# Kernel optimization log

Hardware: AMD Instinct MI355X
Metric: run time of the kernel (lower is better)

Reference implementation:

```python
import jax, jax.numpy as jnp
import numpy as np

D = 512
H = 8
DK = D // H
EPS = 1e-5

def _layer_norm(x, w, b):
    mu = jnp.mean(x, axis=-1, keepdims=True)
    var = jnp.mean(jnp.square(x - mu), axis=-1, keepdims=True)
    return (x - mu) * jax.lax.rsqrt(var + EPS) * w + b

def setup_inputs() -> dict:
    key = jax.random.key(0)
    ks = jax.random.split(key, 16)
    B, S = 4, 2048
    s = 1.0 / np.sqrt(D)
    inp = {
        'q': jax.random.normal(ks[0], (B, S, D), jnp.float32),
        'k': jax.random.normal(ks[1], (B, S, D), jnp.float32),
        'v': jax.random.normal(ks[2], (B, S, D), jnp.float32),
        'mask': jnp.ones((S, S), jnp.int32),
        'pos_k': jax.random.normal(ks[3], (S, S), jnp.float32),
        'ln_w': jnp.ones((D,), jnp.float32),
        'ln_b': jnp.zeros((D,), jnp.float32),
        'Wq': jax.random.uniform(ks[4], (D, D), jnp.float32, -s, s),
        'bq': jax.random.uniform(ks[5], (D,), jnp.float32, -s, s),
        'Wk': jax.random.uniform(ks[6], (D, D), jnp.float32, -s, s),
        'bk': jax.random.uniform(ks[7], (D,), jnp.float32, -s, s),
        'Wv': jax.random.uniform(ks[8], (D, D), jnp.float32, -s, s),
        'bv': jax.random.uniform(ks[9], (D,), jnp.float32, -s, s),
        'Wo': jax.random.uniform(ks[10], (D, D), jnp.float32, -s, s),
        'bo': jax.random.uniform(ks[11], (D,), jnp.float32, -s, s),
    }
    return inp

def reference(q, k, v, mask, pos_k, ln_w, ln_b, Wq, bq, Wk, bk, Wv, bv, Wo, bo):
    B, S, _ = q.shape
    # shared LayerNorm on q, k, v
    qn = _layer_norm(q, ln_w, ln_b)
    kn = _layer_norm(k, ln_w, ln_b)
    vn = _layer_norm(v, ln_w, ln_b)
    # projections -> [B, H, S, DK]
    qh = (qn @ Wq.T + bq).reshape(B, S, H, DK).transpose(0, 2, 1, 3)
    kh = (kn @ Wk.T + bk).reshape(B, S, H, DK).transpose(0, 2, 1, 3)
    vh = (vn @ Wv.T + bv).reshape(B, S, H, DK).transpose(0, 2, 1, 3)
    scores = jnp.einsum('bhqd,bhkd->bhqk', qh, kh) / np.sqrt(DK)
    scores = scores + pos_k[None, None, :S, :S]
    scores = jnp.where(mask[None, None] == 0, -jnp.inf, scores)
    attn = jax.nn.softmax(scores, axis=-1)  # dropout is identity in eval
    x = jnp.einsum('bhqk,bhkd->bhqd', attn, vh).transpose(0, 2, 1, 3).reshape(B, S, D)
    out = x @ Wo.T + bo
    return out, attn
```

## Files before the change

kernel.cpp:

```cpp
#include <hip/hip_runtime.h>


typedef __bf16 bf16;
typedef __attribute__((ext_vector_type(8))) __bf16 bfv8;
typedef __attribute__((ext_vector_type(4))) __bf16 bfv4;
typedef __attribute__((ext_vector_type(2))) __bf16 bfv2;
typedef __attribute__((ext_vector_type(4))) float  f32x4;
typedef __attribute__((ext_vector_type(2))) float  f32x2;

static constexpr int Dm = 512, Hh = 8, Sq = 2048, Bb = 4;
static constexpr int BS = Bb * Sq;

__device__ __forceinline__ f32x4 mfma16(bfv8 a, bfv8 b, f32x4 c) {
  return __builtin_amdgcn_mfma_f32_16x16x32_bf16(a, b, c, 0, 0, 0);
}

__global__ __launch_bounds__(256) void posT_kernel(
    const float* __restrict__ pos, const int* __restrict__ mask,
    float* __restrict__ posT) {
  __shared__ float tile[32][33];
  int i0 = blockIdx.y * 32, j0 = blockIdx.x * 32;
  int tx = threadIdx.x & 31, ty = threadIdx.x >> 5;
#pragma unroll
  for (int rr = 0; rr < 32; rr += 8) {
    int i = i0 + ty + rr, j = j0 + tx;
    float pv = pos[(size_t)i * Sq + j];
    int   mv = mask[(size_t)i * Sq + j];
    tile[ty + rr][tx] = mv ? pv : -1e30f;
  }
  __syncthreads();
#pragma unroll
  for (int rr = 0; rr < 32; rr += 8) {
    int j = j0 + ty + rr, i = i0 + tx;
    posT[(size_t)j * Sq + i] = tile[tx][ty + rr];
  }
}

__global__ __launch_bounds__(256) void ln_kernel(
    const float* __restrict__ q, const float* __restrict__ k,
    const float* __restrict__ v, const float* __restrict__ w,
    const float* __restrict__ bia, bf16* __restrict__ qn,
    bf16* __restrict__ kn, bf16* __restrict__ vn) {
  int wv = threadIdx.x >> 6, lane = threadIdx.x & 63;
  int row = blockIdx.x * 4 + wv;
  int which = blockIdx.y;
  const float* src = which == 0 ? q : (which == 1 ? k : v);
  bf16* dst        = which == 0 ? qn : (which == 1 ? kn : vn);

  f32x4 x0 = *(const f32x4*)(src + (size_t)row * Dm + lane * 8);
  f32x4 x1 = *(const f32x4*)(src + (size_t)row * Dm + lane * 8 + 4);
  float xf[8], s1 = 0.f, s2 = 0.f;
#pragma unroll
  for (int i = 0; i < 4; i++) { xf[i] = x0[i]; xf[4 + i] = x1[i]; }
#pragma unroll
  for (int i = 0; i < 8; i++) { s1 += xf[i]; s2 += xf[i] * xf[i]; }
#pragma unroll
  for (int m = 1; m < 64; m <<= 1) { s1 += __shfl_xor(s1, m, 64); s2 += __shfl_xor(s2, m, 64); }
  float mu = s1 * (1.0f / 512.0f);
  float var = s2 * (1.0f / 512.0f) - mu * mu;
  float rs = rsqrtf(var + 1e-5f);
  f32x4 w0 = *(const f32x4*)(w + lane * 8);
  f32x4 w1 = *(const f32x4*)(w + lane * 8 + 4);
  f32x4 b0 = *(const f32x4*)(bia + lane * 8);
  f32x4 b1 = *(const f32x4*)(bia + lane * 8 + 4);
  bfv8 o;
#pragma unroll
  for (int i = 0; i < 4; i++) {
    o[i]     = (bf16)((xf[i] - mu) * rs * w0[i] + b0[i]);
    o[4 + i] = (bf16)((xf[4 + i] - mu) * rs * w1[i] + b1[i]);
  }
  *(bfv8*)(dst + (size_t)row * Dm + lane * 8) = o;
}

__global__ __launch_bounds__(256) void gemm_bt(
    const bf16* __restrict__ A, const float* __restrict__ W,
    const float* __restrict__ bias, bf16* __restrict__ outb,
    float* __restrict__ outf, int mode) {
  __shared__ __align__(16) bf16 As[64][72];
  __shared__ __align__(16) bf16 Bs[64][72];
  int m0 = blockIdx.x * 64, n0 = blockIdx.y * 64;
  int tid = threadIdx.x;
  int wv = tid >> 6, lane = tid & 63;
  int wm = (wv & 1) * 32, wn = (wv >> 1) * 32;
  int r16 = lane & 15, quad = lane >> 4;
  int lr = tid >> 2, sc = (tid & 3) * 16;

  f32x4 acc[2][2] = {};
  const bf16*  Ap = A + (size_t)(m0 + lr) * 512 + sc;
  const float* Wp = W + (size_t)(n0 + lr) * 512 + sc;

  for (int k0 = 0; k0 < 512; k0 += 64) {
    bfv8 a0 = *(const bfv8*)(Ap + k0);
    bfv8 a1 = *(const bfv8*)(Ap + k0 + 8);
    f32x4 w0 = *(const f32x4*)(Wp + k0);
    f32x4 w1 = *(const f32x4*)(Wp + k0 + 4);
    f32x4 w2 = *(const f32x4*)(Wp + k0 + 8);
    f32x4 w3 = *(const f32x4*)(Wp + k0 + 12);
    bfv8 bb0, bb1;
#pragma unroll
    for (int i = 0; i < 4; i++) {
      bb0[i] = (bf16)w0[i]; bb0[4 + i] = (bf16)w1[i];
      bb1[i] = (bf16)w2[i]; bb1[4 + i] = (bf16)w3[i];
    }
    __syncthreads();
    *(bfv8*)&As[lr][sc] = a0;  *(bfv8*)&As[lr][sc + 8] = a1;
    *(bfv8*)&Bs[lr][sc] = bb0; *(bfv8*)&Bs[lr][sc + 8] = bb1;
    __syncthreads();
#pragma unroll
    for (int kk = 0; kk < 2; kk++) {
      bfv8 af0 = *(const bfv8*)&As[wm + r16][kk * 32 + quad * 8];
      bfv8 af1 = *(const bfv8*)&As[wm + 16 + r16][kk * 32 + quad * 8];
      bfv8 bf0 = *(const bfv8*)&Bs[wn + r16][kk * 32 + quad * 8];
      bfv8 bf1 = *(const bfv8*)&Bs[wn + 16 + r16][kk * 32 + quad * 8];
      acc[0][0] = mfma16(af0, bf0, acc[0][0]);
      acc[0][1] = mfma16(af0, bf1, acc[0][1]);
      acc[1][0] = mfma16(af1, bf0, acc[1][0]);
      acc[1][1] = mfma16(af1, bf1, acc[1][1]);
    }
  }

#pragma unroll
  for (int nt = 0; nt < 2; nt++) {
    int n = n0 + wn + nt * 16 + r16;
    float bb = bias[n];
#pragma unroll
    for (int mt = 0; mt < 2; mt++) {
#pragma unroll
      for (int r = 0; r < 4; r++) {
        int m = m0 + wm + mt * 16 + quad * 4 + r;
        float o = acc[mt][nt][r] + bb;
        int bb_ = m >> 11, s = m & 2047, hh = n >> 6, dd = n & 63;
        if (mode == 0)
          outb[(((size_t)(bb_ * Hh + hh)) * Sq + s) * 64 + dd] = (bf16)o;
        else if (mode == 1)
          outb[(((size_t)(bb_ * Hh + hh)) * 64 + dd) * Sq + s] = (bf16)o;
        else
          outf[(size_t)m * 512 + n] = o;
      }
    }
  }
}

__global__ __launch_bounds__(512, 4) void attn_kernel(
    const bf16* __restrict__ qh, const bf16* __restrict__ kh,
    const bf16* __restrict__ vT, const float* __restrict__ posT,
    float* __restrict__ attn, bf16* __restrict__ xout) {
  __shared__ float smax[8][16];
  __shared__ float ssum[8][16];
  __shared__ __align__(16) bf16 Pbuf[8][16][136];
  __shared__ __align__(16) float xred[8][16][64];

  const int tid = threadIdx.x;
  const int wv = tid >> 6, lane = tid & 63;
  const int r16 = lane & 15, quad = lane >> 4;
  const int strip = blockIdx.x, h = blockIdx.y, b = blockIdx.z;
  const int bh = b * Hh + h;
  const int r0 = strip * 16;
  const int c0 = wv * 256;

  const bf16* qbase = qh + (size_t)bh * Sq * 64;
  const bf16* kbase = kh + (size_t)bh * Sq * 64;
  const bf16* vbase = vT + (size_t)bh * 64 * Sq;

  bfv8 aq0 = *(const bfv8*)(qbase + (size_t)(r0 + r16) * 64 + quad * 8);
  bfv8 aq1 = *(const bfv8*)(qbase + (size_t)(r0 + r16) * 64 + 32 + quad * 8);

  f32x4 acc[16];
#pragma unroll
  for (int t = 0; t < 16; t++) {
    const bf16* kp = kbase + (size_t)(c0 + t * 16 + r16) * 64 + quad * 8;
    bfv8 kb0 = *(const bfv8*)kp;
    bfv8 kb1 = *(const bfv8*)(kp + 32);
    f32x4 z = {0.f, 0.f, 0.f, 0.f};
    z = mfma16(aq0, kb0, z);
    z = mfma16(aq1, kb1, z);
    acc[t] = z;
  }

  float mx[4] = {-1e30f, -1e30f, -1e30f, -1e30f};
#pragma unroll
  for (int t = 0; t < 16; t++) {
    int colg = c0 + t * 16 + r16;
    f32x4 pk = *(const f32x4*)(posT + (size_t)colg * Sq + r0 + quad * 4);
#pragma unroll
    for (int r = 0; r < 4; r++) {
      float s = acc[t][r] * 0.125f + pk[r];
      acc[t][r] = s;
      mx[r] = fmaxf(mx[r], s);
    }
  }
#pragma unroll
  for (int m = 1; m < 16; m <<= 1)
#pragma unroll
    for (int r = 0; r < 4; r++) mx[r] = fmaxf(mx[r], __shfl_xor(mx[r], m, 64));

  float sm[4] = {0.f, 0.f, 0.f, 0.f};
#pragma unroll
  for (int t = 0; t < 16; t++)
#pragma unroll
    for (int r = 0; r < 4; r++) {
      float e = __expf(acc[t][r] - mx[r]);
      acc[t][r] = e;
      sm[r] += e;
    }
#pragma unroll
  for (int m = 1; m < 16; m <<= 1)
#pragma unroll
    for (int r = 0; r < 4; r++) sm[r] += __shfl_xor(sm[r], m, 64);

  if (r16 == 0) {
#pragma unroll
    for (int r = 0; r < 4; r++) {
      smax[wv][quad * 4 + r] = mx[r];
      ssum[wv][quad * 4 + r] = sm[r];
    }
  }
  __syncthreads();

  float comb[4];
#pragma unroll
  for (int r = 0; r < 4; r++) {
    int row = quad * 4 + r;
    float M = smax[0][row];
#pragma unroll
    for (int w = 1; w < 8; w++) M = fmaxf(M, smax[w][row]);
    float S = 0.f;
#pragma unroll
    for (int w = 0; w < 8; w++) S += ssum[w][row] * __expf(smax[w][row] - M);
    comb[r] = __expf(mx[r] - M) / S;
  }

  f32x4 xacc[4] = {};
#pragma unroll
  for (int c = 0; c < 2; c++) {
#pragma unroll
    for (int tt = 0; tt < 8; tt++) {
      int t = c * 8 + tt;
      int colg = c0 + t * 16 + r16;
#pragma unroll
      for (int r = 0; r < 4; r++) {
        float p = acc[t][r] * comb[r];
        Pbuf[wv][quad * 4 + r][tt * 16 + r16] = (bf16)p;
        __builtin_nontemporal_store(
            p, attn + ((size_t)bh * Sq + r0 + quad * 4 + r) * Sq + colg);
      }
    }
#pragma unroll
    for (int ks = 0; ks < 4; ks++) {
      bfv8 af = *(const bfv8*)&Pbuf[wv][r16][ks * 32 + quad * 8];
      int key0 = c0 + c * 128 + ks * 32;
#pragma unroll
      for (int nt = 0; nt < 4; nt++) {
        bfv8 bvv = *(const bfv8*)(vbase + (size_t)(nt * 16 + r16) * Sq + key0 + quad * 8);
        xacc[nt] = mfma16(af, bvv, xacc[nt]);
      }
    }
  }

#pragma unroll
  for (int nt = 0; nt < 4; nt++)
#pragma unroll
    for (int r = 0; r < 4; r++)
      xred[wv][quad * 4 + r][nt * 16 + r16] = xacc[nt][r];
  __syncthreads();
  {
    int row = tid >> 5, d2 = (tid & 31) * 2;
    f32x2 s = {0.f, 0.f};
#pragma unroll
    for (int w = 0; w < 8; w++) s += *(const f32x2*)&xred[w][row][d2];
    bfv2 o;
    o[0] = (bf16)s[0];
    o[1] = (bf16)s[1];
    *(bfv2*)(xout + ((size_t)(b * Sq + r0 + row)) * 512 + h * 64 + d2) = o;
  }
}

extern "C" void kernel_launch(void* const* d_in, const int* in_sizes, int n_in,
                              void* d_out, int out_size, void* d_ws,
                              size_t ws_size, hipStream_t stream) {
  const float* q    = (const float*)d_in[0];
  const float* k    = (const float*)d_in[1];
  const float* v    = (const float*)d_in[2];
  const int*   mask = (const int*)d_in[3];
  const float* pos  = (const float*)d_in[4];
  const float* lnw  = (const float*)d_in[5];
  const float* lnb  = (const float*)d_in[6];
  const float* Wq   = (const float*)d_in[7];
  const float* bq   = (const float*)d_in[8];
  const float* Wk   = (const float*)d_in[9];
  const float* bk   = (const float*)d_in[10];
  const float* Wv   = (const float*)d_in[11];
  const float* bv   = (const float*)d_in[12];
  const float* Wo   = (const float*)d_in[13];
  const float* bo   = (const float*)d_in[14];

  const size_t NE = (size_t)Bb * Sq * Dm;
  if (ws_size < 64ull * 1024 * 1024) return;

  char* wsb = (char*)d_ws;
  float* posT = (float*)wsb;
  bf16* qn   = (bf16*)(wsb + 16ull * 1024 * 1024);
  bf16* kn   = (bf16*)(wsb + 24ull * 1024 * 1024);
  bf16* vn   = (bf16*)(wsb + 32ull * 1024 * 1024);
  bf16* qhp  = (bf16*)(wsb + 40ull * 1024 * 1024);
  bf16* khp  = (bf16*)(wsb + 48ull * 1024 * 1024);
  bf16* vhT  = (bf16*)(wsb + 56ull * 1024 * 1024);
  bf16* xbuf = qn;

  float* out  = (float*)d_out;
  float* attn = out + NE;

  posT_kernel<<<dim3(Sq / 32, Sq / 32), 256, 0, stream>>>(pos, mask, posT);
  ln_kernel<<<dim3(BS / 4, 3), 256, 0, stream>>>(q, k, v, lnw, lnb, qn, kn, vn);
  gemm_bt<<<dim3(BS / 64, Dm / 64), 256, 0, stream>>>(qn, Wq, bq, qhp, nullptr, 0);
  gemm_bt<<<dim3(BS / 64, Dm / 64), 256, 0, stream>>>(kn, Wk, bk, khp, nullptr, 0);
  gemm_bt<<<dim3(BS / 64, Dm / 64), 256, 0, stream>>>(vn, Wv, bv, vhT, nullptr, 1);
  attn_kernel<<<dim3(Sq / 16, Hh, Bb), 512, 0, stream>>>(qhp, khp, vhT, posT,
                                                         attn, xbuf);
  gemm_bt<<<dim3(BS / 64, Dm / 64), 256, 0, stream>>>(xbuf, Wo, bo, nullptr, out, 2);
}
```

Baseline: 962.9 us.

## Batch QKV projections, alias attention LDS buffers, remap block order, drop nontemporal stores

```diff
diff --git a/kernel.cpp b/kernel.cpp
--- a/kernel.cpp
+++ b/kernel.cpp
@@ -72,13 +72,12 @@
   *(bfv8*)(dst + (size_t)row * Dm + lane * 8) = o;
 }
 
-__global__ __launch_bounds__(256) void gemm_bt(
+__device__ __forceinline__ void gemm_body(
     const bf16* __restrict__ A, const float* __restrict__ W,
     const float* __restrict__ bias, bf16* __restrict__ outb,
-    float* __restrict__ outf, int mode) {
+    float* __restrict__ outf, int mode, int m0, int n0) {
   __shared__ __align__(16) bf16 As[64][72];
   __shared__ __align__(16) bf16 Bs[64][72];
-  int m0 = blockIdx.x * 64, n0 = blockIdx.y * 64;
   int tid = threadIdx.x;
   int wv = tid >> 6, lane = tid & 63;
   int wm = (wv & 1) * 32, wn = (wv >> 1) * 32;
@@ -141,20 +140,48 @@
   }
 }
 
+__global__ __launch_bounds__(256) void gemm_proj(
+    const bf16* __restrict__ qn, const bf16* __restrict__ kn,
+    const bf16* __restrict__ vn, const float* __restrict__ Wq,
+    const float* __restrict__ Wk, const float* __restrict__ Wv,
+    const float* __restrict__ bq, const float* __restrict__ bk,
+    const float* __restrict__ bv, bf16* __restrict__ qhp,
+    bf16* __restrict__ khp, bf16* __restrict__ vhT) {
+  int z = blockIdx.z;
+  const bf16*  A    = z == 0 ? qn : (z == 1 ? kn : vn);
+  const float* W    = z == 0 ? Wq : (z == 1 ? Wk : Wv);
+  const float* bias = z == 0 ? bq : (z == 1 ? bk : bv);
+  bf16*        outb = z == 0 ? qhp : (z == 1 ? khp : vhT);
+  int mode = (z == 2) ? 1 : 0;
+  gemm_body(A, W, bias, outb, nullptr, mode, blockIdx.x * 64, blockIdx.y * 64);
+}
+
+__global__ __launch_bounds__(256) void gemm_bt(
+    const bf16* __restrict__ A, const float* __restrict__ W,
+    const float* __restrict__ bias, bf16* __restrict__ outb,
+    float* __restrict__ outf, int mode) {
+  gemm_body(A, W, bias, outb, outf, mode, blockIdx.x * 64, blockIdx.y * 64);
+}
+
 __global__ __launch_bounds__(512, 4) void attn_kernel(
     const bf16* __restrict__ qh, const bf16* __restrict__ kh,
     const bf16* __restrict__ vT, const float* __restrict__ posT,
     float* __restrict__ attn, bf16* __restrict__ xout) {
   __shared__ float smax[8][16];
   __shared__ float ssum[8][16];
-  __shared__ __align__(16) bf16 Pbuf[8][16][136];
-  __shared__ __align__(16) float xred[8][16][64];
+  __shared__ __align__(16) char upool[8 * 16 * 136 * 2];
+  auto Pbuf = reinterpret_cast<bf16(*)[16][136]>(upool);
+  auto xred = reinterpret_cast<float(*)[16][64]>(upool);
 
   const int tid = threadIdx.x;
   const int wv = tid >> 6, lane = tid & 63;
   const int r16 = lane & 15, quad = lane >> 4;
-  const int strip = blockIdx.x, h = blockIdx.y, b = blockIdx.z;
-  const int bh = b * Hh + h;
+
+  const int bid = blockIdx.x;
+  const int nbid = (bid & 7) * 512 + (bid >> 3);
+  const int bh = nbid >> 7;
+  const int strip = nbid & 127;
+  const int b = bh >> 3, h = bh & 7;
   const int r0 = strip * 16;
   const int c0 = wv * 256;
 
@@ -241,8 +268,7 @@
       for (int r = 0; r < 4; r++) {
         float p = acc[t][r] * comb[r];
         Pbuf[wv][quad * 4 + r][tt * 16 + r16] = (bf16)p;
-        __builtin_nontemporal_store(
-            p, attn + ((size_t)bh * Sq + r0 + quad * 4 + r) * Sq + colg);
+        attn[((size_t)bh * Sq + r0 + quad * 4 + r) * Sq + colg] = p;
       }
     }
 #pragma unroll
@@ -257,6 +283,7 @@
     }
   }
 
+  __syncthreads();
 #pragma unroll
   for (int nt = 0; nt < 4; nt++)
 #pragma unroll
@@ -312,10 +339,9 @@
 
   posT_kernel<<<dim3(Sq / 32, Sq / 32), 256, 0, stream>>>(pos, mask, posT);
   ln_kernel<<<dim3(BS / 4, 3), 256, 0, stream>>>(q, k, v, lnw, lnb, qn, kn, vn);
-  gemm_bt<<<dim3(BS / 64, Dm / 64), 256, 0, stream>>>(qn, Wq, bq, qhp, nullptr, 0);
-  gemm_bt<<<dim3(BS / 64, Dm / 64), 256, 0, stream>>>(kn, Wk, bk, khp, nullptr, 0);
-  gemm_bt<<<dim3(BS / 64, Dm / 64), 256, 0, stream>>>(vn, Wv, bv, vhT, nullptr, 1);
-  attn_kernel<<<dim3(Sq / 16, Hh, Bb), 512, 0, stream>>>(qhp, khp, vhT, posT,
-                                                         attn, xbuf);
+  gemm_proj<<<dim3(BS / 64, Dm / 64, 3), 256, 0, stream>>>(
+      qn, kn, vn, Wq, Wk, Wv, bq, bk, bv, qhp, khp, vhT);
+  attn_kernel<<<dim3((Sq / 16) * Hh * Bb), 512, 0, stream>>>(qhp, khp, vhT,
+                                                             posT, attn, xbuf);
   gemm_bt<<<dim3(BS / 64, Dm / 64), 256, 0, stream>>>(xbuf, Wo, bo, nullptr, out, 2);
 }
```

Result: no change. 947.4 us (-1.6%).
